# Performance work log

Measured on AMD Instinct MI355X. Metric: run time of the kernel, lower is better.

The kernel has to match this reference:

```python
import jax, jax.numpy as jnp
import numpy as np

B, N, E = 2, 2048, 1024
H = 16
NE = 16                                  # num experts
TOPN = 2
CAP = max(4, int(N * 1.25 / NE))         # expert capacity = 160 (train, cf=1.25)
HFF = int(E * 4 * 2 / 3)                 # 2730, Expert_alt hidden
EPS = 1e-9
BLOCK = 64                               # spatial block size for block-causal mask


def setup_inputs():
    key = jax.random.key(0)
    ks = jax.random.split(key, 16)
    def nrm(k, shape, s=0.02):
        return jax.random.normal(k, shape, dtype=jnp.float32) * s
    # block-causal mask (tril over time blocks, repeat_interleave spatially); True = masked
    blk = np.tril(np.ones((N // BLOCK, N // BLOCK)))
    blk = np.repeat(np.repeat(blk, BLOCK, axis=0), BLOCK, axis=1)
    attn_mask = jnp.asarray(~blk.astype(bool))
    return dict(
        x=jax.random.normal(ks[0], (B, N, E), jnp.float32),
        attn_mask=attn_mask,
        in_proj_w=nrm(ks[1], (3 * E, E)),
        in_proj_b=jnp.zeros((3 * E,), jnp.float32),
        out_proj_w=nrm(ks[2], (E, E)),
        out_proj_b=jnp.zeros((E,), jnp.float32),
        rms_gamma=jnp.ones((E,), jnp.float32),
        gate_w=nrm(ks[3], (NE, E)),
        ln_g=jnp.ones((NE, E), jnp.float32),
        ln_b=jnp.zeros((NE, E), jnp.float32),
        w1=nrm(ks[4], (NE, HFF, E)),
        b1=jnp.zeros((NE, HFF), jnp.float32),
        w2=nrm(ks[5], (NE, E, HFF)),
        b2=jnp.zeros((NE, E), jnp.float32),
        route_unif=jax.random.uniform(ks[6], (TOPN, B, N), jnp.float32),
    )


def _layernorm(t, g, b, eps=1e-5):
    mu = t.mean(-1, keepdims=True)
    var = ((t - mu) ** 2).mean(-1, keepdims=True)
    return (t - mu) * jax.lax.rsqrt(var + eps) * g + b


def _forward(x, attn_mask, in_proj_w, in_proj_b, out_proj_w, out_proj_b,
             rms_gamma, gate_w, ln_g, ln_b, w1, b1, w2, b2, route_unif):
    dh = E // H
    # ---- multi-head self-attention (torch nn.MultiheadAttention math) ----
    qkv = x @ in_proj_w.T + in_proj_b                       # (B,N,3E)
    q, k, v = jnp.split(qkv, 3, axis=-1)
    to_heads = lambda t: t.reshape(B, N, H, dh).transpose(0, 2, 1, 3)
    q, k, v = to_heads(q), to_heads(k), to_heads(v)
    scores = jnp.einsum('bhqd,bhkd->bhqk', q, k) / jnp.sqrt(jnp.float32(dh))
    scores = jnp.where(attn_mask[None, None], -jnp.inf, scores)
    attn = jax.nn.softmax(scores, axis=-1)
    o = jnp.einsum('bhqk,bhkd->bhqd', attn, v).transpose(0, 2, 1, 3).reshape(B, N, E)
    o = o @ out_proj_w.T + out_proj_b
    y = o + x                                               # residual around MHA

    # ---- SparseMoEBlock: RMSNorm prenorm -> MoE -> residual ----
    residual = y
    nrm = y / jnp.clip(jnp.linalg.norm(y, axis=-1, keepdims=True), 1e-12)
    moe_in = nrm * jnp.sqrt(jnp.float32(E)) * rms_gamma

    # ---- top-2 gating (st-moe TopNGating, training mode) ----
    logits = moe_in @ gate_w.T                              # (B,N,NE)
    raw_gates = jax.nn.softmax(logits, axis=-1)
    gates_v, gate_idx = jax.lax.top_k(raw_gates, TOPN)      # (B,N,2)
    gates = jnp.moveaxis(gates_v, -1, 0)                    # (2,B,N)
    gate_idx = jnp.moveaxis(gate_idx, -1, 0)
    one_hot_idx = jax.nn.one_hot(gate_idx, NE, dtype=jnp.float32)  # (2,B,N,NE)
    mask = one_hot_idx
    mask_1 = mask[0]
    denom = jnp.clip(gates.sum(0, keepdims=True), EPS)
    gates = gates / denom
    threshold = jnp.array([EPS, 0.2], jnp.float32)[:, None, None]
    should_route = route_unif < gates / jnp.clip(threshold, EPS)
    should_route = should_route.at[0].set(True)             # always route to top-1
    mask = mask * should_route[..., None].astype(jnp.float32)
    mask_cumsum = jnp.cumsum(mask, axis=-2) - mask          # exclusive cumsum over N

    positions, masks_k = [], []
    prev = jnp.zeros((B, 1, NE), jnp.float32)
    capf = jnp.float32(CAP)
    for n_ in range(TOPN):
        pos = (mask_cumsum[n_] + prev) * mask[n_]           # (B,N,NE)
        mk = mask[n_] * (pos < capf).astype(jnp.float32)    # drop over-capacity
        prev = prev + mk.sum(axis=-2, keepdims=True)
        positions.append(pos.sum(-1))                       # (B,N)
        masks_k.append(mk)
    positions = jnp.stack(positions)                        # (2,B,N)
    mask = jnp.stack(masks_k)
    mask_flat = mask.sum(-1)                                # (2,B,N)
    gates = gates * mask_flat

    pos_oh = jax.nn.one_hot(positions.astype(jnp.int32), CAP, dtype=jnp.float32)  # (2,B,N,CAP)
    combine = jnp.einsum('kbn,kbn,kbne,kbnc->bnec', gates, mask_flat, one_hot_idx, pos_oh)
    dispatch_hard = (combine > 0).astype(jnp.float32)
    dispatch = dispatch_hard + combine - jax.lax.stop_gradient(combine)  # straight-through

    # ---- aux losses ----
    density_1 = mask_1.mean(-2)                             # (B,NE)
    density_proxy = raw_gates.mean(-2)
    balance_loss = (density_proxy * density_1).mean() * jnp.float32(NE ** 2)
    router_z_loss = jnp.mean(jax.nn.logsumexp(logits, axis=-1) ** 2)

    # ---- dispatch -> experts -> combine ----
    expert_inputs = jnp.einsum('bnd,bnec->ebcd', moe_in, dispatch)  # (NE,B,CAP,E)

    def expert_fn(g, bl, W1, B1, W2, B2, xin):
        h = _layernorm(xin, g, bl)
        h = h @ W1.T + B1
        h = jnp.where(h >= 0, h, 0.01 * h)                  # LeakyReLU(0.01)
        return h @ W2.T + B2

    expert_out = jax.vmap(expert_fn)(ln_g, ln_b, w1, b1, w2, b2, expert_inputs)
    moe_out = jnp.einsum('bnec,ebcd->bnd', combine, expert_out)

    out = moe_out + residual
    total_aux = balance_loss * 0.01 + router_z_loss * 0.001
    return out, total_aux, balance_loss, router_z_loss


def reference(x, attn_mask, in_proj_w, in_proj_b, out_proj_w, out_proj_b,
              rms_gamma, gate_w, ln_g, ln_b, w1, b1, w2, b2, route_unif):
    return _forward(x, attn_mask, in_proj_w, in_proj_b, out_proj_w, out_proj_b,
                    rms_gamma, gate_w, ln_g, ln_b, w1, b1, w2, b2, route_unif)
```

## Files before the change

kernel.cpp:

```cpp
#include <hip/hip_runtime.h>
#include <hip/hip_bf16.h>
#include <cstdint>

#define NSEQ  2048
#define BSZ   2
#define NTOK  4096
#define EDIM  1024
#define NEXP  16
#define CAPC  160
#define HFF_R 2730
#define HFF_P 2752

typedef __bf16 bf16_t;
typedef __bf16 bf16x8 __attribute__((ext_vector_type(8)));
typedef __bf16 bf16x4 __attribute__((ext_vector_type(4)));
typedef float  f32x4  __attribute__((ext_vector_type(4)));
typedef unsigned int uint32;

__device__ inline bf16x8 zero8() {
    bf16x8 v;
#pragma unroll
    for (int i = 0; i < 8; i++) v[i] = (bf16_t)0.f;
    return v;
}
__device__ inline bf16x8 pack8(float4 a, float4 b) {
    bf16x8 v;
    v[0]=(bf16_t)a.x; v[1]=(bf16_t)a.y; v[2]=(bf16_t)a.z; v[3]=(bf16_t)a.w;
    v[4]=(bf16_t)b.x; v[5]=(bf16_t)b.y; v[6]=(bf16_t)b.z; v[7]=(bf16_t)b.w;
    return v;
}
struct hl_t { bf16_t h, l; };
__device__ inline hl_t split1(float f) {
    hl_t r;
    r.h = (bf16_t)f;
    r.l = (bf16_t)(f - (float)r.h);
    return r;
}

template <int EPI, int C_SPLIT>
__global__ __launch_bounds__(256) void gemm_split(
    const float* __restrict__ A, const float* __restrict__ Bw,
    const float* __restrict__ bias, const float* __restrict__ resid,
    bf16_t* __restrict__ Chi, bf16_t* __restrict__ Clo, float* __restrict__ Cf,
    int M, int N, int K, int scale_cut, float scale_val)
{
    __shared__ __align__(16) bf16_t Ah[128 * 40], Al[128 * 40];
    __shared__ __align__(16) bf16_t Bh[128 * 40], Bl[128 * 40];
    const int t = threadIdx.x;
    const int m0 = blockIdx.y * 128, n0 = blockIdx.x * 128;
    const int lane = t & 63, l15 = lane & 15, lg = lane >> 4;
    const int wid = t >> 6, wm = wid >> 1, wn = wid & 1;
    const int srow = t >> 1, skc = (t & 1) * 16;

    f32x4 acc[4][4];
    const f32x4 zf = {0.f, 0.f, 0.f, 0.f};
#pragma unroll
    for (int i = 0; i < 4; i++)
#pragma unroll
        for (int j = 0; j < 4; j++) acc[i][j] = zf;

    float4 sa0, sa1, sa2, sa3, sb0, sb1, sb2, sb3;
    auto LOADAB = [&](int k0) {
        const float* ap = A + (long)(m0 + srow) * K + k0 + skc;
        sa0 = *(const float4*)ap;       sa1 = *(const float4*)(ap + 4);
        sa2 = *(const float4*)(ap + 8); sa3 = *(const float4*)(ap + 12);
        const float* bp = Bw + (long)(n0 + srow) * K + k0 + skc;
        sb0 = *(const float4*)bp;       sb1 = *(const float4*)(bp + 4);
        sb2 = *(const float4*)(bp + 8); sb3 = *(const float4*)(bp + 12);
    };
    auto WRITEAB = [&]() {
        float av[16], bv[16];
        *(float4*)&av[0] = sa0; *(float4*)&av[4] = sa1;
        *(float4*)&av[8] = sa2; *(float4*)&av[12] = sa3;
        *(float4*)&bv[0] = sb0; *(float4*)&bv[4] = sb1;
        *(float4*)&bv[8] = sb2; *(float4*)&bv[12] = sb3;
        bf16x8 h0, h1, l0, l1;
#pragma unroll
        for (int i = 0; i < 8; i++) {
            hl_t a = split1(av[i]);      h0[i] = a.h; l0[i] = a.l;
            hl_t b = split1(av[8 + i]);  h1[i] = b.h; l1[i] = b.l;
        }
        *(bf16x8*)&Ah[srow * 40 + skc] = h0; *(bf16x8*)&Ah[srow * 40 + skc + 8] = h1;
        *(bf16x8*)&Al[srow * 40 + skc] = l0; *(bf16x8*)&Al[srow * 40 + skc + 8] = l1;
#pragma unroll
        for (int i = 0; i < 8; i++) {
            hl_t a = split1(bv[i]);      h0[i] = a.h; l0[i] = a.l;
            hl_t b = split1(bv[8 + i]);  h1[i] = b.h; l1[i] = b.l;
        }
        *(bf16x8*)&Bh[srow * 40 + skc] = h0; *(bf16x8*)&Bh[srow * 40 + skc + 8] = h1;
        *(bf16x8*)&Bl[srow * 40 + skc] = l0; *(bf16x8*)&Bl[srow * 40 + skc + 8] = l1;
    };

    LOADAB(0);
    for (int k0 = 0; k0 < K; k0 += 32) {
        WRITEAB();
        __syncthreads();
        if (k0 + 32 < K) LOADAB(k0 + 32);
        bf16x8 amh[4], aml[4], bnh[4], bnl[4];
#pragma unroll
        for (int i = 0; i < 4; i++) {
            int base = (wm * 64 + i * 16 + l15) * 40 + lg * 8;
            amh[i] = *(const bf16x8*)&Ah[base];
            aml[i] = *(const bf16x8*)&Al[base];
        }
#pragma unroll
        for (int j = 0; j < 4; j++) {
            int base = (wn * 64 + j * 16 + l15) * 40 + lg * 8;
            bnh[j] = *(const bf16x8*)&Bh[base];
            bnl[j] = *(const bf16x8*)&Bl[base];
        }
        __builtin_amdgcn_s_setprio(1);
#pragma unroll
        for (int i = 0; i < 4; i++)
#pragma unroll
            for (int j = 0; j < 4; j++) {
                acc[i][j] = __builtin_amdgcn_mfma_f32_16x16x32_bf16(amh[i], bnh[j], acc[i][j], 0, 0, 0);
                acc[i][j] = __builtin_amdgcn_mfma_f32_16x16x32_bf16(amh[i], bnl[j], acc[i][j], 0, 0, 0);
                acc[i][j] = __builtin_amdgcn_mfma_f32_16x16x32_bf16(aml[i], bnh[j], acc[i][j], 0, 0, 0);
            }
        __builtin_amdgcn_s_setprio(0);
        __syncthreads();
    }

#pragma unroll
    for (int i = 0; i < 4; i++) {
        int mgb = m0 + wm * 64 + i * 16 + lg * 4;
#pragma unroll
        for (int j = 0; j < 4; j++) {
            int ng = n0 + wn * 64 + j * 16 + l15;
            float bval = bias[ng];
#pragma unroll
            for (int r = 0; r < 4; r++) {
                int mg = mgb + r;
                float val = acc[i][j][r] + bval;
                if (scale_cut > 0 && ng < scale_cut) val *= scale_val;
                if (EPI == 2) val += resid[(long)mg * N + ng];
                long idx = (long)mg * N + ng;
                if (C_SPLIT) {
                    bf16_t hi = (bf16_t)val;
                    Chi[idx] = hi;
                    Clo[idx] = (bf16_t)(val - (float)hi);
                } else {
                    Cf[idx] = val;
                }
            }
        }
    }
}

template <int EPI, int C_BF16>
__global__ __launch_bounds__(256) void gemm_ffn(
    const bf16_t* __restrict__ Av, const float* __restrict__ Bw,
    const float* __restrict__ bias, void* __restrict__ Cv,
    int N, int Nwr, int KA, int KB,
    long sAe, long sBe, long sBiasE, long sCe, int ldc)
{
    __shared__ __align__(16) bf16_t Alds[320 * 72];
    __shared__ __align__(16) bf16_t Blds[64 * 72];
    const int id = blockIdx.x;
    const int e = id & 15, nt = id >> 4;
    const int n0 = nt * 64;
    const int t = threadIdx.x;
    const int lane = t & 63, l15 = lane & 15, lg = lane >> 4;
    const int wid = t >> 6, wm = wid >> 1, wn = wid & 1;
    const int srow = t >> 2, scol = (t & 3) * 16;

    f32x4 acc[10][2];
    const f32x4 zf = {0.f, 0.f, 0.f, 0.f};
#pragma unroll
    for (int i = 0; i < 10; i++)
#pragma unroll
        for (int j = 0; j < 2; j++) acc[i][j] = zf;

    bf16x8 sa[5][2];
    float4 sb0, sb1, sb2, sb3;
    const float4 zf4 = {0.f, 0.f, 0.f, 0.f};
    auto LOADA = [&](int k0) {
        const bf16_t* abase = Av + (long)e * sAe + k0 + scol;
#pragma unroll
        for (int p = 0; p < 5; p++) {
            const bf16_t* ap = abase + (long)(srow + 64 * p) * KA;
            sa[p][0] = *(const bf16x8*)ap;
            sa[p][1] = *(const bf16x8*)(ap + 8);
        }
    };
    auto LOADB = [&](int k0) {
        int ng = n0 + srow;
        if (ng < N) {
            const float* bp = Bw + (long)e * sBe + (long)ng * KB + k0 + scol;
            if (k0 + 64 <= KB) {
                sb0 = *(const float4*)bp;       sb1 = *(const float4*)(bp + 4);
                sb2 = *(const float4*)(bp + 8); sb3 = *(const float4*)(bp + 12);
            } else {
                float v[16];
#pragma unroll
                for (int i = 0; i < 16; i++) {
                    int kk = k0 + scol + i;
                    v[i] = (kk < KB) ? bp[i] : 0.f;
                }
                sb0 = *(float4*)&v[0];  sb1 = *(float4*)&v[4];
                sb2 = *(float4*)&v[8];  sb3 = *(float4*)&v[12];
            }
        } else {
            sb0 = zf4; sb1 = zf4; sb2 = zf4; sb3 = zf4;
        }
    };
    auto WRITEAB = [&]() {
#pragma unroll
        for (int p = 0; p < 5; p++) {
            *(bf16x8*)&Alds[(srow + 64 * p) * 72 + scol]     = sa[p][0];
            *(bf16x8*)&Alds[(srow + 64 * p) * 72 + scol + 8] = sa[p][1];
        }
        *(bf16x8*)&Blds[srow * 72 + scol]     = pack8(sb0, sb1);
        *(bf16x8*)&Blds[srow * 72 + scol + 8] = pack8(sb2, sb3);
    };

    LOADA(0); LOADB(0);
    for (int k0 = 0; k0 < KA; k0 += 64) {
        WRITEAB();
        __syncthreads();
        if (k0 + 64 < KA) { LOADA(k0 + 64); LOADB(k0 + 64); }
#pragma unroll
        for (int ks = 0; ks < 2; ks++) {
            bf16x8 bn[2];
#pragma unroll
            for (int j = 0; j < 2; j++)
                bn[j] = *(const bf16x8*)&Blds[(wn * 32 + j * 16 + l15) * 72 + ks * 32 + lg * 8];
            bf16x8 am[10];
#pragma unroll
            for (int i = 0; i < 10; i++)
                am[i] = *(const bf16x8*)&Alds[(wm * 160 + i * 16 + l15) * 72 + ks * 32 + lg * 8];
            __builtin_amdgcn_s_setprio(1);
#pragma unroll
            for (int i = 0; i < 10; i++)
#pragma unroll
                for (int j = 0; j < 2; j++)
                    acc[i][j] = __builtin_amdgcn_mfma_f32_16x16x32_bf16(am[i], bn[j], acc[i][j], 0, 0, 0);
            __builtin_amdgcn_s_setprio(0);
        }
        __syncthreads();
    }

    const float* biasp = bias + (long)e * sBiasE;
#pragma unroll
    for (int i = 0; i < 10; i++) {
        int mgb = wm * 160 + i * 16 + lg * 4;
#pragma unroll
        for (int j = 0; j < 2; j++) {
            int ng = n0 + wn * 32 + j * 16 + l15;
            if (ng < Nwr) {
                float bval = (ng < N) ? biasp[ng] : 0.f;
#pragma unroll
                for (int r = 0; r < 4; r++) {
                    int mg = mgb + r;
                    float val = acc[i][j][r] + bval;
                    if (EPI == 1) val = (val >= 0.f) ? val : 0.01f * val;
                    if (ng >= N) val = 0.f;
                    long cidx = (long)e * sCe + (long)mg * ldc + ng;
                    if (C_BF16) ((bf16_t*)Cv)[cidx] = (bf16_t)val;
                    else        ((float*)Cv)[cidx] = val;
                }
            }
        }
    }
}

__global__ __launch_bounds__(256) void attn_split(const bf16_t* __restrict__ qh,
                                                  const bf16_t* __restrict__ ql,
                                                  float* __restrict__ o)
{
    __shared__ __align__(16) bf16_t KhS[64 * 72], KlS[64 * 72];
    __shared__ __align__(16) bf16_t VhS[64 * 72], VlS[64 * 72];
    __shared__ __align__(16) bf16_t PhS[4][2][16 * 72], PlS[4][2][16 * 72];

    const int id = blockIdx.x;
    const int x  = id & 7;
    const int s  = id >> 3;
    const int b  = s >> 5;
    const int s5 = s & 31;
    const int qraw = s5 & 15;
    const int h  = x + 8 * (s5 >> 4);
    const int qt = b ? (15 - qraw) : qraw;
    const int nkb = 2 * qt + 2;

    const int t = threadIdx.x, wid = t >> 6, lane = t & 63, l15 = lane & 15, lg = lane >> 4;
    const int krow = t >> 2, kdc = (t & 3) * 16;
    const int vk = t & 63, vdg = (t >> 6) * 16;
    const long kvb = (long)(b * NSEQ) * 3072 + 1024 + h * 64;
    const f32x4 zf = {0.f, 0.f, 0.f, 0.f};

    const long qo0 = (long)(b * NSEQ + qt * 128 + wid * 16 + l15) * 3072 + h * 64 + lg * 8;
    const long qo1 = qo0 + (long)64 * 3072;
    bf16x8 q0h0 = *(const bf16x8*)(qh + qo0), q0h1 = *(const bf16x8*)(qh + qo0 + 32);
    bf16x8 q0l0 = *(const bf16x8*)(ql + qo0), q0l1 = *(const bf16x8*)(ql + qo0 + 32);
    bf16x8 q1h0 = *(const bf16x8*)(qh + qo1), q1h1 = *(const bf16x8*)(qh + qo1 + 32);
    bf16x8 q1l0 = *(const bf16x8*)(ql + qo1), q1l1 = *(const bf16x8*)(ql + qo1 + 32);

    f32x4 O0[4], O1[4];
    float m0r[4], l0r[4], m1r[4], l1r[4];
#pragma unroll
    for (int r = 0; r < 4; r++) {
        O0[r] = zf; O1[r] = zf;
        m0r[r] = -1e30f; l0r[r] = 0.f; m1r[r] = -1e30f; l1r[r] = 0.f;
    }

    bf16x8 skh0, skh1, skl0, skl1, svh0, svh1, svl0, svl1;
    auto LOADKV = [&](int kb) {
        long ko = kvb + (long)(kb * 64 + krow) * 3072 + kdc;
        skh0 = *(const bf16x8*)(qh + ko); skh1 = *(const bf16x8*)(qh + ko + 8);
        skl0 = *(const bf16x8*)(ql + ko); skl1 = *(const bf16x8*)(ql + ko + 8);
        long vo = kvb + 1024 + (long)(kb * 64 + vk) * 3072 + vdg;
        svh0 = *(const bf16x8*)(qh + vo); svh1 = *(const bf16x8*)(qh + vo + 8);
        svl0 = *(const bf16x8*)(ql + vo); svl1 = *(const bf16x8*)(ql + vo + 8);
    };
    auto WRITEKV = [&]() {
        *(bf16x8*)&KhS[krow * 72 + kdc]     = skh0;
        *(bf16x8*)&KhS[krow * 72 + kdc + 8] = skh1;
        *(bf16x8*)&KlS[krow * 72 + kdc]     = skl0;
        *(bf16x8*)&KlS[krow * 72 + kdc + 8] = skl1;
#pragma unroll
        for (int i = 0; i < 8; i++) {
            VhS[(vdg + i) * 72 + vk]     = svh0[i];
            VhS[(vdg + 8 + i) * 72 + vk] = svh1[i];
            VlS[(vdg + i) * 72 + vk]     = svl0[i];
            VlS[(vdg + 8 + i) * 72 + vk] = svl1[i];
        }
    };

    LOADKV(0);
    for (int kb = 0; kb < nkb; kb++) {
        __syncthreads();
        WRITEKV();
        __syncthreads();
        if (kb + 1 < nkb) LOADKV(kb + 1);
        const bool g0a = (kb < nkb - 1);
        f32x4 s0[4], s1[4];
        __builtin_amdgcn_s_setprio(1);
#pragma unroll
        for (int ks = 0; ks < 4; ks++) {
            int base = (ks * 16 + l15) * 72 + lg * 8;
            bf16x8 kh0 = *(const bf16x8*)&KhS[base];
            bf16x8 kh1 = *(const bf16x8*)&KhS[base + 32];
            bf16x8 kl0 = *(const bf16x8*)&KlS[base];
            bf16x8 kl1 = *(const bf16x8*)&KlS[base + 32];
            f32x4 a = zf;
            a = __builtin_amdgcn_mfma_f32_16x16x32_bf16(q1h0, kh0, a, 0, 0, 0);
            a = __builtin_amdgcn_mfma_f32_16x16x32_bf16(q1h1, kh1, a, 0, 0, 0);
            a = __builtin_amdgcn_mfma_f32_16x16x32_bf16(q1h0, kl0, a, 0, 0, 0);
            a = __builtin_amdgcn_mfma_f32_16x16x32_bf16(q1h1, kl1, a, 0, 0, 0);
            a = __builtin_amdgcn_mfma_f32_16x16x32_bf16(q1l0, kh0, a, 0, 0, 0);
            a = __builtin_amdgcn_mfma_f32_16x16x32_bf16(q1l1, kh1, a, 0, 0, 0);
            s1[ks] = a;
            f32x4 c = zf;
            if (g0a) {
                c = __builtin_amdgcn_mfma_f32_16x16x32_bf16(q0h0, kh0, c, 0, 0, 0);
                c = __builtin_amdgcn_mfma_f32_16x16x32_bf16(q0h1, kh1, c, 0, 0, 0);
                c = __builtin_amdgcn_mfma_f32_16x16x32_bf16(q0h0, kl0, c, 0, 0, 0);
                c = __builtin_amdgcn_mfma_f32_16x16x32_bf16(q0h1, kl1, c, 0, 0, 0);
                c = __builtin_amdgcn_mfma_f32_16x16x32_bf16(q0l0, kh0, c, 0, 0, 0);
                c = __builtin_amdgcn_mfma_f32_16x16x32_bf16(q0l1, kh1, c, 0, 0, 0);
            }
            s0[ks] = c;
        }
        __builtin_amdgcn_s_setprio(0);
        {
            float alpha[4];
#pragma unroll
            for (int r = 0; r < 4; r++) {
                float mt = fmaxf(fmaxf(s1[0][r], s1[1][r]), fmaxf(s1[2][r], s1[3][r]));
#pragma unroll
                for (int m = 1; m < 16; m <<= 1) mt = fmaxf(mt, __shfl_xor(mt, m));
                float mn = fmaxf(m1r[r], mt);
                alpha[r] = __expf(m1r[r] - mn);
                m1r[r] = mn;
            }
            float ladd[4] = {0.f, 0.f, 0.f, 0.f};
#pragma unroll
            for (int ks = 0; ks < 4; ks++)
#pragma unroll
                for (int r = 0; r < 4; r++) {
                    float p = __expf(s1[ks][r] - m1r[r]);
                    s1[ks][r] = p;
                    ladd[r] += p;
                }
#pragma unroll
            for (int r = 0; r < 4; r++) {
#pragma unroll
                for (int m = 1; m < 16; m <<= 1) ladd[r] += __shfl_xor(ladd[r], m);
                l1r[r] = l1r[r] * alpha[r] + ladd[r];
            }
#pragma unroll
            for (int sb = 0; sb < 4; sb++)
#pragma unroll
                for (int r = 0; r < 4; r++) O1[sb][r] *= alpha[r];
            bf16_t* pwh = &PhS[wid][1][0];
            bf16_t* pwl = &PlS[wid][1][0];
#pragma unroll
            for (int ks = 0; ks < 4; ks++)
#pragma unroll
                for (int r = 0; r < 4; r++) {
                    hl_t pv = split1(s1[ks][r]);
                    pwh[(lg * 4 + r) * 72 + ks * 16 + l15] = pv.h;
                    pwl[(lg * 4 + r) * 72 + ks * 16 + l15] = pv.l;
                }
        }
        if (g0a) {
            float alpha[4];
#pragma unroll
            for (int r = 0; r < 4; r++) {
                float mt = fmaxf(fmaxf(s0[0][r], s0[1][r]), fmaxf(s0[2][r], s0[3][r]));
#pragma unroll
                for (int m = 1; m < 16; m <<= 1) mt = fmaxf(mt, __shfl_xor(mt, m));
                float mn = fmaxf(m0r[r], mt);
                alpha[r] = __expf(m0r[r] - mn);
                m0r[r] = mn;
            }
            float ladd[4] = {0.f, 0.f, 0.f, 0.f};
#pragma unroll
            for (int ks = 0; ks < 4; ks++)
#pragma unroll
                for (int r = 0; r < 4; r++) {
                    float p = __expf(s0[ks][r] - m0r[r]);
                    s0[ks][r] = p;
                    ladd[r] += p;
                }
#pragma unroll
            for (int r = 0; r < 4; r++) {
#pragma unroll
                for (int m = 1; m < 16; m <<= 1) ladd[r] += __shfl_xor(ladd[r], m);
                l0r[r] = l0r[r] * alpha[r] + ladd[r];
            }
#pragma unroll
            for (int sb = 0; sb < 4; sb++)
#pragma unroll
                for (int r = 0; r < 4; r++) O0[sb][r] *= alpha[r];
            bf16_t* pwh = &PhS[wid][0][0];
            bf16_t* pwl = &PlS[wid][0][0];
#pragma unroll
            for (int ks = 0; ks < 4; ks++)
#pragma unroll
                for (int r = 0; r < 4; r++) {
                    hl_t pv = split1(s0[ks][r]);
                    pwh[(lg * 4 + r) * 72 + ks * 16 + l15] = pv.h;
                    pwl[(lg * 4 + r) * 72 + ks * 16 + l15] = pv.l;
                }
        }
        __builtin_amdgcn_s_setprio(1);
#pragma unroll
        for (int kst = 0; kst < 2; kst++) {
            bf16x8 pf1h = *(const bf16x8*)&PhS[wid][1][l15 * 72 + kst * 32 + lg * 8];
            bf16x8 pf1l = *(const bf16x8*)&PlS[wid][1][l15 * 72 + kst * 32 + lg * 8];
            bf16x8 pf0h, pf0l;
            if (g0a) {
                pf0h = *(const bf16x8*)&PhS[wid][0][l15 * 72 + kst * 32 + lg * 8];
                pf0l = *(const bf16x8*)&PlS[wid][0][l15 * 72 + kst * 32 + lg * 8];
            }
#pragma unroll
            for (int sb = 0; sb < 4; sb++) {
                int base = (sb * 16 + l15) * 72 + kst * 32 + lg * 8;
                bf16x8 vfh = *(const bf16x8*)&VhS[base];
                bf16x8 vfl = *(const bf16x8*)&VlS[base];
                O1[sb] = __builtin_amdgcn_mfma_f32_16x16x32_bf16(pf1h, vfh, O1[sb], 0, 0, 0);
                O1[sb] = __builtin_amdgcn_mfma_f32_16x16x32_bf16(pf1h, vfl, O1[sb], 0, 0, 0);
                O1[sb] = __builtin_amdgcn_mfma_f32_16x16x32_bf16(pf1l, vfh, O1[sb], 0, 0, 0);
                if (g0a) {
                    O0[sb] = __builtin_amdgcn_mfma_f32_16x16x32_bf16(pf0h, vfh, O0[sb], 0, 0, 0);
                    O0[sb] = __builtin_amdgcn_mfma_f32_16x16x32_bf16(pf0h, vfl, O0[sb], 0, 0, 0);
                    O0[sb] = __builtin_amdgcn_mfma_f32_16x16x32_bf16(pf0l, vfh, O0[sb], 0, 0, 0);
                }
            }
        }
        __builtin_amdgcn_s_setprio(0);
    }
#pragma unroll
    for (int sb = 0; sb < 4; sb++)
#pragma unroll
        for (int r = 0; r < 4; r++) {
            int qg0 = qt * 128 + wid * 16 + lg * 4 + r;
            int col = h * 64 + sb * 16 + l15;
            o[(long)(b * NSEQ + qg0) * 1024 + col] = O0[sb][r] / l0r[r];
            o[(long)(b * NSEQ + qg0 + 64) * 1024 + col] = O1[sb][r] / l1r[r];
        }
}

__global__ __launch_bounds__(256) void rmsnorm_kernel(const float* __restrict__ y,
                                                      const float* __restrict__ gamma,
                                                      float* __restrict__ moe)
{
    long base = (long)blockIdx.x * 1024;
    float4 v = ((const float4*)(y + base))[threadIdx.x];
    float ss = v.x * v.x + v.y * v.y + v.z * v.z + v.w * v.w;
#pragma unroll
    for (int m = 32; m; m >>= 1) ss += __shfl_xor(ss, m);
    __shared__ float ls[4];
    if ((threadIdx.x & 63) == 0) ls[threadIdx.x >> 6] = ss;
    __syncthreads();
    float tot = ls[0] + ls[1] + ls[2] + ls[3];
    float sc = 32.0f / fmaxf(sqrtf(tot), 1e-12f);
    float4 g = ((const float4*)gamma)[threadIdx.x];
    float4 ov;
    ov.x = v.x * sc * g.x; ov.y = v.y * sc * g.y; ov.z = v.z * sc * g.z; ov.w = v.w * sc * g.w;
    ((float4*)(moe + base))[threadIdx.x] = ov;
}

__global__ __launch_bounds__(256) void gating_kernel(
    const float* __restrict__ moe, const float* __restrict__ gw,
    const float* __restrict__ runif, uint32* __restrict__ tokpack,
    float* __restrict__ tokg, float* __restrict__ acc)
{
    const int wid = threadIdx.x >> 6, lane = threadIdx.x & 63;
    const int tk = blockIdx.x * 4 + wid;
    const int b = tk >> 11, n = tk & 2047;
    float xv[16];
    const float4* xr4 = (const float4*)(moe + (long)tk * 1024 + lane * 16);
#pragma unroll
    for (int i = 0; i < 4; i++) {
        float4 v = xr4[i];
        xv[4 * i] = v.x; xv[4 * i + 1] = v.y; xv[4 * i + 2] = v.z; xv[4 * i + 3] = v.w;
    }
    float logit[16];
#pragma unroll
    for (int e = 0; e < 16; e++) {
        const float4* wr4 = (const float4*)(gw + e * 1024 + lane * 16);
        float p = 0.f;
#pragma unroll
        for (int i = 0; i < 4; i++) {
            float4 w = wr4[i];
            p = fmaf(xv[4 * i], w.x, p);     p = fmaf(xv[4 * i + 1], w.y, p);
            p = fmaf(xv[4 * i + 2], w.z, p); p = fmaf(xv[4 * i + 3], w.w, p);
        }
#pragma unroll
        for (int m = 1; m < 64; m <<= 1) p += __shfl_xor(p, m);
        logit[e] = p;
    }
    int e0 = 0; float t0 = logit[0];
#pragma unroll
    for (int e = 1; e < 16; e++) if (logit[e] > t0) { t0 = logit[e]; e0 = e; }
    int e1 = (e0 == 0) ? 1 : 0; float t1 = logit[e1];
#pragma unroll
    for (int e = 0; e < 16; e++) if (e != e0 && logit[e] > t1) { t1 = logit[e]; e1 = e; }
    float g0n = 1.f / (1.f + __expf(t1 - t0));
    float g1n = 1.f / (1.f + __expf(t0 - t1));
    int sr1 = (runif[(long)(BSZ + b) * NSEQ + n] < g1n / 0.2f) ? 1 : 0;
    float mx = t0, sum = 0.f, raw[16];
#pragma unroll
    for (int e = 0; e < 16; e++) { raw[e] = __expf(logit[e] - mx); sum += raw[e]; }
    float inv = 1.f / sum;
    float lse = mx + __logf(sum);
    if (lane == 0) {
        tokpack[tk] = (uint32)e0 | ((uint32)e1 << 4) | ((uint32)sr1 << 8);
        tokg[2 * tk] = g0n; tokg[2 * tk + 1] = g1n;
        atomicAdd(&acc[32 + b * 16 + e0], 1.0f);
        atomicAdd(&acc[64], lse * lse);
    }
    if (lane < 16) atomicAdd(&acc[b * 16 + lane], raw[lane] * inv);
}

__global__ __launch_bounds__(512) void scan_kernel(const uint32* __restrict__ tokpack,
                                                   uint32* __restrict__ r0,
                                                   uint32* __restrict__ r1,
                                                   int* __restrict__ prev)
{
    const int b = blockIdx.x, t = threadIdx.x;
    const int wv = t >> 6, lane = t & 63;
    uint32 toks[4];
    *(uint4*)toks = ((const uint4*)(tokpack + b * NSEQ))[t];

    uint32 c0[8], c1[8];
#pragma unroll
    for (int j = 0; j < 8; j++) { c0[j] = 0u; c1[j] = 0u; }
#pragma unroll
    for (int i = 0; i < 4; i++) {
        uint32 p = toks[i];
        uint32 e0 = p & 15, e1 = (p >> 4) & 15, sr1 = (p >> 8) & 1;
        uint32 inc0 = 1u << ((e0 & 1) * 16);
        uint32 inc1 = sr1 << ((e1 & 1) * 16);
#pragma unroll
        for (int j = 0; j < 8; j++) {
            c0[j] += ((e0 >> 1) == (uint32)j) ? inc0 : 0u;
            c1[j] += ((e1 >> 1) == (uint32)j) ? inc1 : 0u;
        }
    }
    uint32 i0[8], i1[8];
#pragma unroll
    for (int j = 0; j < 8; j++) { i0[j] = c0[j]; i1[j] = c1[j]; }
#pragma unroll
    for (int off = 1; off < 64; off <<= 1) {
#pragma unroll
        for (int j = 0; j < 8; j++) {
            uint32 u0 = __shfl_up(i0[j], off);
            uint32 u1 = __shfl_up(i1[j], off);
            if (lane >= off) { i0[j] += u0; i1[j] += u1; }
        }
    }
    __shared__ uint32 wsum0[8][8], wsum1[8][8];
    if (lane == 63) {
#pragma unroll
        for (int j = 0; j < 8; j++) { wsum0[wv][j] = i0[j]; wsum1[wv][j] = i1[j]; }
    }
    __syncthreads();
    uint32 b0[8], b1[8];
#pragma unroll
    for (int j = 0; j < 8; j++) {
        uint32 s0 = 0u, s1 = 0u;
#pragma unroll
        for (int w = 0; w < 8; w++) {
            s0 += (w < wv) ? wsum0[w][j] : 0u;
            s1 += (w < wv) ? wsum1[w][j] : 0u;
        }
        b0[j] = s0 + i0[j] - c0[j];
        b1[j] = s1 + i1[j] - c1[j];
    }
    if (t == 0) {
#pragma unroll
        for (int j = 0; j < 8; j++) {
            uint32 tot = 0u;
#pragma unroll
            for (int w = 0; w < 8; w++) tot += wsum0[w][j];
            int tlo = (int)(tot & 0xffffu), thi = (int)(tot >> 16);
            prev[b * 16 + 2 * j]     = tlo < CAPC ? tlo : CAPC;
            prev[b * 16 + 2 * j + 1] = thi < CAPC ? thi : CAPC;
        }
    }
    uint32* rr0 = r0 + b * NSEQ + t * 4;
    uint32* rr1 = r1 + b * NSEQ + t * 4;
#pragma unroll
    for (int i = 0; i < 4; i++) {
        uint32 p = toks[i];
        uint32 e0 = p & 15, e1 = (p >> 4) & 15, sr1 = (p >> 8) & 1;
        uint32 sh0 = (e0 & 1) * 16, sh1 = (e1 & 1) * 16;
        uint32 w0 = 0u, w1 = 0u;
#pragma unroll
        for (int j = 0; j < 8; j++) {
            w0 += ((e0 >> 1) == (uint32)j) ? b0[j] : 0u;
            w1 += ((e1 >> 1) == (uint32)j) ? b1[j] : 0u;
        }
        uint32 s0 = (w0 >> sh0) & 0xffffu;
        uint32 s1v = (w1 >> sh1) & 0xffffu;
        uint32 kept = (s0 < CAPC) ? 1u : 0u;
        rr0[i] = e0 | (kept << 4) | (s0 << 5);
        rr1[i] = e1 | (sr1 << 4) | (s1v << 5);
        uint32 inc0 = 1u << sh0;
        uint32 inc1 = sr1 << sh1;
#pragma unroll
        for (int j = 0; j < 8; j++) {
            b0[j] += ((e0 >> 1) == (uint32)j) ? inc0 : 0u;
            b1[j] += ((e1 >> 1) == (uint32)j) ? inc1 : 0u;
        }
    }
}

__global__ __launch_bounds__(256) void gather_kernel(
    const float* __restrict__ moe, const uint32* __restrict__ r0,
    const uint32* __restrict__ r1, const int* __restrict__ prev,
    float* __restrict__ ein)
{
    int tk = blockIdx.x, b = tk >> 11;
    float4 v = ((const float4*)(moe + (long)tk * 1024))[threadIdx.x];
    uint32 a = r0[tk];
    if ((a >> 4) & 1) {
        long row = ((long)(a & 15) * 2 + b) * CAPC + (int)(a >> 5);
        ((float4*)(ein + row * 1024))[threadIdx.x] = v;
    }
    uint32 c = r1[tk];
    {
        int e = c & 15, sr1 = (c >> 4) & 1;
        int slot = (int)(c >> 5) + prev[b * 16 + e];
        if (sr1 && slot < CAPC) {
            long row = ((long)e * 2 + b) * CAPC + slot;
            ((float4*)(ein + row * 1024))[threadIdx.x] = v;
        }
    }
}

__global__ __launch_bounds__(256) void expert_ln_kernel(
    const float* __restrict__ ein, const float* __restrict__ g,
    const float* __restrict__ bb, bf16_t* __restrict__ eout)
{
    int row = blockIdx.x, e = row / (BSZ * CAPC);
    long base = (long)row * 1024;
    float4 v = ((const float4*)(ein + base))[threadIdx.x];
    float s = v.x + v.y + v.z + v.w;
    float ss = v.x * v.x + v.y * v.y + v.z * v.z + v.w * v.w;
#pragma unroll
    for (int m = 32; m; m >>= 1) { s += __shfl_xor(s, m); ss += __shfl_xor(ss, m); }
    __shared__ float l1[4], l2[4];
    if ((threadIdx.x & 63) == 0) { l1[threadIdx.x >> 6] = s; l2[threadIdx.x >> 6] = ss; }
    __syncthreads();
    float st = l1[0] + l1[1] + l1[2] + l1[3];
    float sst = l2[0] + l2[1] + l2[2] + l2[3];
    float mu = st * (1.f / 1024.f);
    float var = sst * (1.f / 1024.f) - mu * mu;
    float rstd = rsqrtf(var + 1e-5f);
    int d = threadIdx.x * 4;
    float4 gg = *(const float4*)(g + e * 1024 + d);
    float4 bv = *(const float4*)(bb + e * 1024 + d);
    bf16x4 ov;
    ov[0] = (bf16_t)((v.x - mu) * rstd * gg.x + bv.x);
    ov[1] = (bf16_t)((v.y - mu) * rstd * gg.y + bv.y);
    ov[2] = (bf16_t)((v.z - mu) * rstd * gg.z + bv.z);
    ov[3] = (bf16_t)((v.w - mu) * rstd * gg.w + bv.w);
    *(bf16x4*)(eout + base + d) = ov;
}

__global__ __launch_bounds__(256) void combine_kernel(
    const float* __restrict__ y, const float* __restrict__ eout,
    const uint32* __restrict__ r0, const uint32* __restrict__ r1,
    const float* __restrict__ tokg, const int* __restrict__ prev,
    float* __restrict__ out)
{
    int tk = blockIdx.x, b = tk >> 11;
    uint32 a = r0[tk], c = r1[tk];
    int k0f = (a >> 4) & 1;
    float w0 = k0f ? tokg[2 * tk] : 0.f;
    long row0 = ((long)(a & 15) * 2 + b) * CAPC + (int)(a >> 5);
    int e1 = c & 15;
    int slot1 = (int)(c >> 5) + prev[b * 16 + e1];
    int k1f = (((c >> 4) & 1) && slot1 < CAPC) ? 1 : 0;
    float w1 = k1f ? tokg[2 * tk + 1] : 0.f;
    long row1 = ((long)e1 * 2 + b) * CAPC + slot1;
    int i = threadIdx.x;
    float4 vy = ((const float4*)(y + (long)tk * 1024))[i];
    float4 a0 = {0.f, 0.f, 0.f, 0.f}, a1 = {0.f, 0.f, 0.f, 0.f};
    if (k0f) a0 = ((const float4*)(eout + row0 * 1024))[i];
    if (k1f) a1 = ((const float4*)(eout + row1 * 1024))[i];
    float4 ov;
    ov.x = vy.x + w0 * a0.x + w1 * a1.x;
    ov.y = vy.y + w0 * a0.y + w1 * a1.y;
    ov.z = vy.z + w0 * a0.z + w1 * a1.z;
    ov.w = vy.w + w0 * a0.w + w1 * a1.w;
    ((float4*)(out + (long)tk * 1024))[i] = ov;
}

__global__ void zero_acc_kernel(float* acc)
{
    if (threadIdx.x < 65) acc[threadIdx.x] = 0.f;
}

__global__ void finalize_kernel(const float* __restrict__ acc, float* __restrict__ tail)
{
    int t = threadIdx.x;
    float v = (t < 32) ? acc[t] * acc[32 + t] : 0.f;
#pragma unroll
    for (int m = 1; m < 64; m <<= 1) v += __shfl_xor(v, m);
    if (t == 0) {
        float bal = v * (8.0f / (2048.f * 2048.f));
        float z = acc[64] / 4096.f;
        tail[0] = 0.01f * bal + 0.001f * z;
        tail[1] = bal;
        tail[2] = z;
    }
}

extern "C" void kernel_launch(void* const* d_in, const int* in_sizes, int n_in,
                              void* d_out, int out_size, void* d_ws, size_t ws_size,
                              hipStream_t stream)
{
    (void)in_sizes; (void)n_in; (void)out_size; (void)ws_size;
    const float* x     = (const float*)d_in[0];
    const float* in_w  = (const float*)d_in[2];
    const float* in_b  = (const float*)d_in[3];
    const float* out_w = (const float*)d_in[4];
    const float* out_b = (const float*)d_in[5];
    const float* rg    = (const float*)d_in[6];
    const float* gw    = (const float*)d_in[7];
    const float* lng   = (const float*)d_in[8];
    const float* lnb   = (const float*)d_in[9];
    const float* w1    = (const float*)d_in[10];
    const float* b1    = (const float*)d_in[11];
    const float* w2    = (const float*)d_in[12];
    const float* b2    = (const float*)d_in[13];
    const float* runif = (const float*)d_in[14];
    float* out = (float*)d_out;

    size_t off = 0;
    char* wsb = (char*)d_ws;
    auto take = [&](size_t bytes) -> char* {
        char* p = wsb + off;
        off += (bytes + 255) & ~(size_t)255;
        return p;
    };
    bf16_t* qkvh = (bf16_t*)take((size_t)NTOK * 3072 * 2);
    bf16_t* qkvl = (bf16_t*)take((size_t)NTOK * 3072 * 2);
    float*  obuf = (float*)take((size_t)NTOK * 1024 * 4);
    float*  ybuf = (float*)take((size_t)NTOK * 1024 * 4);
    float*  moe  = (float*)take((size_t)NTOK * 1024 * 4);
    bf16_t* eln  = (bf16_t*)take((size_t)NEXP * BSZ * CAPC * 1024 * 2);
    bf16_t* hbuf = (bf16_t*)take((size_t)NEXP * BSZ * CAPC * HFF_P * 2);
    uint32* tokpack = (uint32*)take(NTOK * 4);
    float*  tokg = (float*)take(NTOK * 8);
    uint32* r0   = (uint32*)take(NTOK * 4);
    uint32* r1   = (uint32*)take(NTOK * 4);
    int*    prev = (int*)take(128);
    float*  acc  = (float*)take(1024);
    float*  ein  = (float*)qkvl;
    float*  eoutv = (float*)qkvh;

    zero_acc_kernel<<<1, 128, 0, stream>>>(acc);

    gemm_split<0, 1><<<dim3(24, 32), 256, 0, stream>>>(
        x, in_w, in_b, nullptr, qkvh, qkvl, nullptr,
        NTOK, 3072, 1024, 1024, 0.125f);

    attn_split<<<dim3(512), 256, 0, stream>>>(qkvh, qkvl, obuf);

    gemm_split<2, 0><<<dim3(8, 32), 256, 0, stream>>>(
        obuf, out_w, out_b, x, nullptr, nullptr, ybuf,
        NTOK, 1024, 1024, 0, 1.0f);

    rmsnorm_kernel<<<NTOK, 256, 0, stream>>>(ybuf, rg, moe);
    gating_kernel<<<NTOK / 4, 256, 0, stream>>>(moe, gw, runif, tokpack, tokg, acc);
    scan_kernel<<<dim3(BSZ), 512, 0, stream>>>(tokpack, r0, r1, prev);
    gather_kernel<<<NTOK, 256, 0, stream>>>(moe, r0, r1, prev, ein);
    expert_ln_kernel<<<NEXP * BSZ * CAPC, 256, 0, stream>>>(ein, lng, lnb, eln);

    gemm_ffn<1, 1><<<dim3(43 * 16), 256, 0, stream>>>(
        eln, w1, b1, hbuf, HFF_R, HFF_P, 1024, 1024,
        (long)320 * 1024, (long)HFF_R * 1024, HFF_R, (long)320 * HFF_P, HFF_P);

    gemm_ffn<0, 0><<<dim3(16 * 16), 256, 0, stream>>>(
        hbuf, w2, b2, eoutv, 1024, 1024, HFF_P, HFF_R,
        (long)320 * HFF_P, (long)1024 * HFF_R, 1024, (long)320 * 1024, 1024);

    combine_kernel<<<NTOK, 256, 0, stream>>>(ybuf, eoutv, r0, r1, tokg, prev, out);
    finalize_kernel<<<1, 64, 0, stream>>>(acc, out + (size_t)NTOK * 1024);
}
```

Baseline: 617.6 us.

## Pre-split GEMM operands into bf16 hi/lo arrays instead of splitting per tile

Adds a standalone split kernel that converts x, in_proj_w and out_proj_w into bf16 hi/lo pairs once per call. The projection GEMMs then load pre-split bf16 tiles directly, which removes the per-tile fp32-to-bf16 split arithmetic from their inner loop. The attention kernel now writes its output already split into hi/lo bf16 for the out-projection. Global traffic per GEMM is unchanged (two bf16 arrays equal one fp32 array), so the gain depends on the split ALU work having been a bottleneck. In exchange it adds three extra launches and extra full passes over x and the weights, and it reuses the eln buffer as scratch for the split x and in_proj_w.

```diff
diff --git a/kernel.cpp b/kernel.cpp
--- a/kernel.cpp
+++ b/kernel.cpp
@@ -37,9 +37,25 @@
     return r;
 }
 
+__global__ __launch_bounds__(256) void split_kernel(const float* __restrict__ src,
+                                                    bf16_t* __restrict__ hi,
+                                                    bf16_t* __restrict__ lo, int n)
+{
+    int i = (blockIdx.x * 256 + threadIdx.x) * 4;
+    if (i >= n) return;
+    float4 v = *(const float4*)(src + i);
+    hl_t a = split1(v.x), b = split1(v.y), c = split1(v.z), d = split1(v.w);
+    bf16x4 h, l;
+    h[0] = a.h; h[1] = b.h; h[2] = c.h; h[3] = d.h;
+    l[0] = a.l; l[1] = b.l; l[2] = c.l; l[3] = d.l;
+    *(bf16x4*)(hi + i) = h;
+    *(bf16x4*)(lo + i) = l;
+}
+
 template <int EPI, int C_SPLIT>
-__global__ __launch_bounds__(256) void gemm_split(
-    const float* __restrict__ A, const float* __restrict__ Bw,
+__global__ __launch_bounds__(256) void gemm_ps(
+    const bf16_t* __restrict__ Ah_, const bf16_t* __restrict__ Al_,
+    const bf16_t* __restrict__ Bh_, const bf16_t* __restrict__ Bl_,
     const float* __restrict__ bias, const float* __restrict__ resid,
     bf16_t* __restrict__ Chi, bf16_t* __restrict__ Clo, float* __restrict__ Cf,
     int M, int N, int K, int scale_cut, float scale_val)
@@ -59,36 +75,20 @@
 #pragma unroll
         for (int j = 0; j < 4; j++) acc[i][j] = zf;
 
-    float4 sa0, sa1, sa2, sa3, sb0, sb1, sb2, sb3;
+    bf16x8 sah0, sah1, sal0, sal1, sbh0, sbh1, sbl0, sbl1;
     auto LOADAB = [&](int k0) {
-        const float* ap = A + (long)(m0 + srow) * K + k0 + skc;
-        sa0 = *(const float4*)ap;       sa1 = *(const float4*)(ap + 4);
-        sa2 = *(const float4*)(ap + 8); sa3 = *(const float4*)(ap + 12);
-        const float* bp = Bw + (long)(n0 + srow) * K + k0 + skc;
-        sb0 = *(const float4*)bp;       sb1 = *(const float4*)(bp + 4);
-        sb2 = *(const float4*)(bp + 8); sb3 = *(const float4*)(bp + 12);
+        long aoff = (long)(m0 + srow) * K + k0 + skc;
+        sah0 = *(const bf16x8*)(Ah_ + aoff); sah1 = *(const bf16x8*)(Ah_ + aoff + 8);
+        sal0 = *(const bf16x8*)(Al_ + aoff); sal1 = *(const bf16x8*)(Al_ + aoff + 8);
+        long boff = (long)(n0 + srow) * K + k0 + skc;
+        sbh0 = *(const bf16x8*)(Bh_ + boff); sbh1 = *(const bf16x8*)(Bh_ + boff + 8);
+        sbl0 = *(const bf16x8*)(Bl_ + boff); sbl1 = *(const bf16x8*)(Bl_ + boff + 8);
     };
     auto WRITEAB = [&]() {
-        float av[16], bv[16];
-        *(float4*)&av[0] = sa0; *(float4*)&av[4] = sa1;
-        *(float4*)&av[8] = sa2; *(float4*)&av[12] = sa3;
-        *(float4*)&bv[0] = sb0; *(float4*)&bv[4] = sb1;
-        *(float4*)&bv[8] = sb2; *(float4*)&bv[12] = sb3;
-        bf16x8 h0, h1, l0, l1;
-#pragma unroll
-        for (int i = 0; i < 8; i++) {
-            hl_t a = split1(av[i]);      h0[i] = a.h; l0[i] = a.l;
-            hl_t b = split1(av[8 + i]);  h1[i] = b.h; l1[i] = b.l;
-        }
-        *(bf16x8*)&Ah[srow * 40 + skc] = h0; *(bf16x8*)&Ah[srow * 40 + skc + 8] = h1;
-        *(bf16x8*)&Al[srow * 40 + skc] = l0; *(bf16x8*)&Al[srow * 40 + skc + 8] = l1;
-#pragma unroll
-        for (int i = 0; i < 8; i++) {
-            hl_t a = split1(bv[i]);      h0[i] = a.h; l0[i] = a.l;
-            hl_t b = split1(bv[8 + i]);  h1[i] = b.h; l1[i] = b.l;
-        }
-        *(bf16x8*)&Bh[srow * 40 + skc] = h0; *(bf16x8*)&Bh[srow * 40 + skc + 8] = h1;
-        *(bf16x8*)&Bl[srow * 40 + skc] = l0; *(bf16x8*)&Bl[srow * 40 + skc + 8] = l1;
+        *(bf16x8*)&Ah[srow * 40 + skc] = sah0; *(bf16x8*)&Ah[srow * 40 + skc + 8] = sah1;
+        *(bf16x8*)&Al[srow * 40 + skc] = sal0; *(bf16x8*)&Al[srow * 40 + skc + 8] = sal1;
+        *(bf16x8*)&Bh[srow * 40 + skc] = sbh0; *(bf16x8*)&Bh[srow * 40 + skc + 8] = sbh1;
+        *(bf16x8*)&Bl[srow * 40 + skc] = sbl0; *(bf16x8*)&Bl[srow * 40 + skc + 8] = sbl1;
     };
 
     LOADAB(0);
@@ -267,7 +267,8 @@
 
 __global__ __launch_bounds__(256) void attn_split(const bf16_t* __restrict__ qh,
                                                   const bf16_t* __restrict__ ql,
-                                                  float* __restrict__ o)
+                                                  bf16_t* __restrict__ oh,
+                                                  bf16_t* __restrict__ ol)
 {
     __shared__ __align__(16) bf16_t KhS[64 * 72], KlS[64 * 72];
     __shared__ __align__(16) bf16_t VhS[64 * 72], VlS[64 * 72];
@@ -478,8 +479,12 @@
         for (int r = 0; r < 4; r++) {
             int qg0 = qt * 128 + wid * 16 + lg * 4 + r;
             int col = h * 64 + sb * 16 + l15;
-            o[(long)(b * NSEQ + qg0) * 1024 + col] = O0[sb][r] / l0r[r];
-            o[(long)(b * NSEQ + qg0 + 64) * 1024 + col] = O1[sb][r] / l1r[r];
+            long i0 = (long)(b * NSEQ + qg0) * 1024 + col;
+            long i1 = (long)(b * NSEQ + qg0 + 64) * 1024 + col;
+            hl_t v0 = split1(O0[sb][r] / l0r[r]);
+            hl_t v1 = split1(O1[sb][r] / l1r[r]);
+            oh[i0] = v0.h; ol[i0] = v0.l;
+            oh[i1] = v1.h; ol[i1] = v1.l;
         }
 }
 
@@ -782,30 +787,41 @@
     };
     bf16_t* qkvh = (bf16_t*)take((size_t)NTOK * 3072 * 2);
     bf16_t* qkvl = (bf16_t*)take((size_t)NTOK * 3072 * 2);
-    float*  obuf = (float*)take((size_t)NTOK * 1024 * 4);
+    bf16_t* oh   = (bf16_t*)take((size_t)NTOK * 1024 * 2);
+    bf16_t* ol   = (bf16_t*)take((size_t)NTOK * 1024 * 2);
     float*  ybuf = (float*)take((size_t)NTOK * 1024 * 4);
     float*  moe  = (float*)take((size_t)NTOK * 1024 * 4);
     bf16_t* eln  = (bf16_t*)take((size_t)NEXP * BSZ * CAPC * 1024 * 2);
     bf16_t* hbuf = (bf16_t*)take((size_t)NEXP * BSZ * CAPC * HFF_P * 2);
+    bf16_t* owh  = (bf16_t*)take((size_t)1024 * 1024 * 2);
+    bf16_t* owl  = (bf16_t*)take((size_t)1024 * 1024 * 2);
     uint32* tokpack = (uint32*)take(NTOK * 4);
     float*  tokg = (float*)take(NTOK * 8);
     uint32* r0   = (uint32*)take(NTOK * 4);
     uint32* r1   = (uint32*)take(NTOK * 4);
     int*    prev = (int*)take(128);
     float*  acc  = (float*)take(1024);
-    float*  ein  = (float*)qkvl;
+    float*  ein   = (float*)qkvl;
     float*  eoutv = (float*)qkvh;
+    bf16_t* xh    = eln;
+    bf16_t* xl    = xh + (size_t)NTOK * 1024;
+    bf16_t* iwh   = xl + (size_t)NTOK * 1024;
+    bf16_t* iwl   = iwh + (size_t)3072 * 1024;
 
     zero_acc_kernel<<<1, 128, 0, stream>>>(acc);
 
-    gemm_split<0, 1><<<dim3(24, 32), 256, 0, stream>>>(
-        x, in_w, in_b, nullptr, qkvh, qkvl, nullptr,
+    split_kernel<<<dim3(NTOK * 1024 / 1024), 256, 0, stream>>>(x, xh, xl, NTOK * 1024);
+    split_kernel<<<dim3(3072 * 1024 / 1024), 256, 0, stream>>>(in_w, iwh, iwl, 3072 * 1024);
+    split_kernel<<<dim3(1024 * 1024 / 1024), 256, 0, stream>>>(out_w, owh, owl, 1024 * 1024);
+
+    gemm_ps<0, 1><<<dim3(24, 32), 256, 0, stream>>>(
+        xh, xl, iwh, iwl, in_b, nullptr, qkvh, qkvl, nullptr,
         NTOK, 3072, 1024, 1024, 0.125f);
 
-    attn_split<<<dim3(512), 256, 0, stream>>>(qkvh, qkvl, obuf);
-
-    gemm_split<2, 0><<<dim3(8, 32), 256, 0, stream>>>(
-        obuf, out_w, out_b, x, nullptr, nullptr, ybuf,
+    attn_split<<<dim3(512), 256, 0, stream>>>(qkvh, qkvl, oh, ol);
+
+    gemm_ps<2, 0><<<dim3(8, 32), 256, 0, stream>>>(
+        oh, ol, owh, owl, out_b, x, nullptr, nullptr, ybuf,
         NTOK, 1024, 1024, 0, 1.0f);
 
     rmsnorm_kernel<<<NTOK, 256, 0, stream>>>(ybuf, rg, moe);
```

Measured after the change: 584.9 us, median of 2. -5.3%, faster.
